# Performance work log

Measured on AMD Instinct MI355X. Metric: run time of the kernel, lower is better.

## Reference

```python
import jax, jax.numpy as jnp
import numpy as np

H = 16          # num_heads
W = 256         # sliding window size
LN_EPS = 1e-6
ROPE_BASE = 10000.0


def layer_norm(x, g, b):
    m = jnp.mean(x, axis=-1, keepdims=True)
    v = jnp.mean((x - m) ** 2, axis=-1, keepdims=True)
    return (x - m) * jax.lax.rsqrt(v + LN_EPS) * g + b


def rope(x):
    # x: [B, S, H, hd]; rotate-half RoPE
    S, hd = x.shape[1], x.shape[-1]
    inv_freq = 1.0 / (ROPE_BASE ** (jnp.arange(0, hd, 2, dtype=jnp.float32) / hd))
    ang = jnp.arange(S, dtype=jnp.float32)[:, None] * inv_freq[None, :]  # [S, hd/2]
    cos = jnp.concatenate([jnp.cos(ang), jnp.cos(ang)], axis=-1)[None, :, None, :]
    sin = jnp.concatenate([jnp.sin(ang), jnp.sin(ang)], axis=-1)[None, :, None, :]
    x1, x2 = jnp.split(x, 2, axis=-1)
    rot = jnp.concatenate([-x2, x1], axis=-1)
    return x * cos + rot * sin


def setup_inputs() -> dict:
    key = jax.random.key(0)
    ks = jax.random.split(key, 12)
    B, S, D, I = 2, 2048, 1024, 4096
    s = 0.02
    return {
        "hidden_states": jax.random.normal(ks[0], (B, S, D), jnp.float32),
        "wq": jax.random.normal(ks[1], (D, D), jnp.float32) * s,
        "wk": jax.random.normal(ks[2], (D, D), jnp.float32) * s,
        "wv": jax.random.normal(ks[3], (D, D), jnp.float32) * s,
        "wo": jax.random.normal(ks[4], (D, D), jnp.float32) * s,
        "w1": jax.random.normal(ks[5], (D, I), jnp.float32) * s,
        "w2": jax.random.normal(ks[6], (I, D), jnp.float32) * s,
        "w3": jax.random.normal(ks[7], (D, I), jnp.float32) * s,
        "ln1_g": jnp.ones((D,), jnp.float32),
        "ln1_b": jnp.zeros((D,), jnp.float32),
        "ln2_g": jnp.ones((D,), jnp.float32),
        "ln2_b": jnp.zeros((D,), jnp.float32),
    }


def reference(hidden_states, wq, wk, wv, wo, w1, w2, w3, ln1_g, ln1_b, ln2_g, ln2_b):
    B, S, D = hidden_states.shape
    hd = D // H

    # --- attention sub-block ---
    residual = hidden_states
    x = layer_norm(hidden_states, ln1_g, ln1_b)
    q = (x @ wq).reshape(B, S, H, hd)
    k = (x @ wk).reshape(B, S, H, hd)
    v = (x @ wv).reshape(B, S, H, hd)
    q, k = rope(q), rope(k)

    scores = jnp.einsum("bqhd,bkhd->bhqk", q, k) / jnp.sqrt(jnp.float32(hd))
    idx = jnp.arange(S)
    rel = idx[:, None] - idx[None, :]          # i - j
    mask = (rel >= 0) & (rel < W)              # causal sliding window
    scores = jnp.where(mask[None, None], scores, jnp.float32(-1e9))
    attn = jax.nn.softmax(scores, axis=-1)
    ctx = jnp.einsum("bhqk,bkhd->bqhd", attn, v).reshape(B, S, D)
    hidden_states = residual + ctx @ wo

    # --- SwiGLU MLP sub-block ---
    residual = hidden_states
    x = layer_norm(hidden_states, ln2_g, ln2_b)
    mlp = (jax.nn.silu(x @ w1) * (x @ w3)) @ w2
    return residual + mlp
```

## Files before the change

### kernel.cpp

```cpp
#include <hip/hip_runtime.h>
#include <hip/hip_bf16.h>

typedef __bf16 bf16_t;
typedef __bf16 bf16x4 __attribute__((ext_vector_type(4)));
typedef __bf16 bf16x8 __attribute__((ext_vector_type(8)));
typedef float f32x4 __attribute__((ext_vector_type(4)));
typedef float f32x16 __attribute__((ext_vector_type(16)));

#define LN_EPS 1e-6f

__device__ __forceinline__ void gl2lds16(const void* g, void* l) {
    __builtin_amdgcn_global_load_lds(
        (const __attribute__((address_space(1))) void*)g,
        (__attribute__((address_space(3))) void*)l, 16, 0, 0);
}

__global__ void transpose_cvt_kernel(const float* __restrict__ in, bf16_t* __restrict__ out,
                                     int R, int C) {
    __shared__ float tile[32][33];
    int tx = threadIdx.x & 31;
    int ty = threadIdx.x >> 5;
    int r0 = blockIdx.y * 32;
    int c0 = blockIdx.x * 32;
#pragma unroll
    for (int i = 0; i < 4; i++) {
        int r = ty + i * 8;
        tile[r][tx] = in[(size_t)(r0 + r) * C + (c0 + tx)];
    }
    __syncthreads();
#pragma unroll
    for (int i = 0; i < 4; i++) {
        int r = ty + i * 8;
        out[(size_t)(c0 + r) * R + (r0 + tx)] = (bf16_t)tile[tx][r];
    }
}

__global__ void ln_kernel(const float* __restrict__ x, const float* __restrict__ g,
                          const float* __restrict__ bb, bf16_t* __restrict__ out, int D) {
    int row = blockIdx.x;
    int t = threadIdx.x;
    const float4* xr = reinterpret_cast<const float4*>(x + (size_t)row * D);
    float4 v = xr[t];
    float s = v.x + v.y + v.z + v.w;
    __shared__ float sbuf[4];
    __shared__ float sbuf2[4];
    int wave = t >> 6, lane = t & 63;
#pragma unroll
    for (int o = 32; o > 0; o >>= 1) s += __shfl_xor(s, o);
    if (lane == 0) sbuf[wave] = s;
    __syncthreads();
    float mean = (sbuf[0] + sbuf[1] + sbuf[2] + sbuf[3]) / (float)D;
    float d0 = v.x - mean, d1 = v.y - mean, d2 = v.z - mean, d3 = v.w - mean;
    float sq = d0 * d0 + d1 * d1 + d2 * d2 + d3 * d3;
#pragma unroll
    for (int o = 32; o > 0; o >>= 1) sq += __shfl_xor(sq, o);
    if (lane == 0) sbuf2[wave] = sq;
    __syncthreads();
    float var = (sbuf2[0] + sbuf2[1] + sbuf2[2] + sbuf2[3]) / (float)D;
    float inv = rsqrtf(var + LN_EPS);
    float4 gv = reinterpret_cast<const float4*>(g)[t];
    float4 bv = reinterpret_cast<const float4*>(bb)[t];
    bf16_t* o0 = out + (size_t)row * D + t * 4;
    o0[0] = (bf16_t)(d0 * inv * gv.x + bv.x);
    o0[1] = (bf16_t)(d1 * inv * gv.y + bv.y);
    o0[2] = (bf16_t)(d2 * inv * gv.z + bv.z);
    o0[3] = (bf16_t)(d3 * inv * gv.w + bv.w);
}

#define BM 128
#define BN 128
#define BKK 32

template <int EPI>
__launch_bounds__(256, 2) __global__
void gemm_kernel(const bf16_t* __restrict__ A, const bf16_t* __restrict__ Bt,
                 float* __restrict__ Cf, const float* __restrict__ aux,
                 const bf16_t* __restrict__ auxb, bf16_t* __restrict__ Cb,
                 int M, int N, int K) {
    __shared__ __align__(16) bf16_t As[BM * BKK];
    __shared__ __align__(16) bf16_t Bs[BN * BKK];
    int t = threadIdx.x;
    int lin = blockIdx.y * gridDim.x + blockIdx.x;
    int gmt = gridDim.y;
    int gw = 8 * gmt;
    int grp = lin / gw;
    int rem = lin - grp * gw;
    int bn = grp * 8 + (rem & 7);
    int bm = rem >> 3;
    int m0 = bm * BM;
    int n0 = bn * BN;
    int wave = t >> 6, lane = t & 63;
    int wm = (wave >> 1) * 64, wn = (wave & 1) * 64;
    int lr = lane & 15;
    int quad = lane >> 4;

    int srow = lane >> 2;
    int scol = (lane & 3) * 8;
    const bf16_t* ag = A + (size_t)(m0 + wave * 16 + srow) * K + scol;
    const bf16_t* bg = Bt + (size_t)(n0 + wave * 16 + srow) * K + scol;
    bf16_t* asl = As + wave * 16 * BKK;
    bf16_t* bsl = Bs + wave * 16 * BKK;
    const size_t rowskip = (size_t)64 * K;

    f32x4 acc[4][4];
#pragma unroll
    for (int mi = 0; mi < 4; mi++)
#pragma unroll
        for (int ni = 0; ni < 4; ni++) acc[mi][ni] = 0.f;

    for (int k0 = 0; k0 < K; k0 += BKK) {
        gl2lds16(ag + k0, asl);
        gl2lds16(ag + k0 + rowskip, asl + 64 * BKK);
        gl2lds16(bg + k0, bsl);
        gl2lds16(bg + k0 + rowskip, bsl + 64 * BKK);
        __syncthreads();
        bf16x8 af[4], bfv[4];
#pragma unroll
        for (int mi = 0; mi < 4; mi++)
            af[mi] = *reinterpret_cast<const bf16x8*>(&As[(wm + mi * 16 + lr) * BKK + quad * 8]);
#pragma unroll
        for (int ni = 0; ni < 4; ni++)
            bfv[ni] = *reinterpret_cast<const bf16x8*>(&Bs[(wn + ni * 16 + lr) * BKK + quad * 8]);
#pragma unroll
        for (int mi = 0; mi < 4; mi++)
#pragma unroll
            for (int ni = 0; ni < 4; ni++)
                acc[mi][ni] = __builtin_amdgcn_mfma_f32_16x16x32_bf16(af[mi], bfv[ni],
                                                                      acc[mi][ni], 0, 0, 0);
        __syncthreads();
    }
#pragma unroll
    for (int mi = 0; mi < 4; mi++) {
#pragma unroll
        for (int ni = 0; ni < 4; ni++) {
#pragma unroll
            for (int j = 0; j < 4; j++) {
                int gm = m0 + wm + mi * 16 + quad * 4 + j;
                int gn = n0 + wn + ni * 16 + lr;
                size_t idx = (size_t)gm * N + gn;
                float val = acc[mi][ni][j];
                if constexpr (EPI == 1) {
                    Cf[idx] = val + aux[idx];
                }
            }
        }
    }
}

#define G2_BM 256
#define G2_BN 128
#define G2_BK 32

template <int EPI>
__launch_bounds__(256, 2) __global__
void gemm2_kernel(const bf16_t* __restrict__ A, const bf16_t* __restrict__ Bt,
                  const bf16_t* __restrict__ auxb, bf16_t* __restrict__ Cb,
                  int M, int N, int K, int lda, int ldb) {
    __shared__ __align__(16) bf16_t As[G2_BM * G2_BK];
    __shared__ __align__(16) bf16_t Bs[G2_BN * G2_BK];
    int t = threadIdx.x;
    int wave = t >> 6, lane = t & 63;
    int m0 = blockIdx.x * G2_BM;
    int n0 = blockIdx.y * G2_BN;
    int koff = blockIdx.z * K;

    int sr = lane >> 2;
    int sq = (lane & 3) ^ (sr & 3);
    const bf16_t* ag = A + (size_t)(m0 + 64 * wave + sr) * lda + koff + sq * 8;
    const bf16_t* bg = Bt + (size_t)(n0 + 32 * wave + sr) * ldb + koff + sq * 8;
    bf16_t* asl = As + (64 * wave) * G2_BK;
    bf16_t* bsl = Bs + (32 * wave) * G2_BK;

    f32x16 acc[2][4];
#pragma unroll
    for (int mi = 0; mi < 2; mi++)
#pragma unroll
        for (int ni = 0; ni < 4; ni++) acc[mi][ni] = 0.f;

    int l31 = lane & 31;
    int lh = lane >> 5;
    int lx = lane & 3;

    for (int k0 = 0; k0 < K; k0 += G2_BK) {
#pragma unroll
        for (int i = 0; i < 4; i++)
            gl2lds16(ag + k0 + (size_t)(16 * i) * lda, asl + (16 * i) * G2_BK);
#pragma unroll
        for (int i = 0; i < 2; i++)
            gl2lds16(bg + k0 + (size_t)(16 * i) * ldb, bsl + (16 * i) * G2_BK);
        __syncthreads();
#pragma unroll
        for (int s = 0; s < 2; s++) {
            int q = 2 * s + lh;
            bf16x8 af[2], bfv[4];
#pragma unroll
            for (int mi = 0; mi < 2; mi++) {
                int row = 64 * wave + mi * 32 + l31;
                af[mi] = *reinterpret_cast<const bf16x8*>(&As[row * G2_BK + (q ^ lx) * 8]);
            }
#pragma unroll
            for (int ni = 0; ni < 4; ni++) {
                int row = ni * 32 + l31;
                bfv[ni] = *reinterpret_cast<const bf16x8*>(&Bs[row * G2_BK + (q ^ lx) * 8]);
            }
#pragma unroll
            for (int mi = 0; mi < 2; mi++)
#pragma unroll
                for (int ni = 0; ni < 4; ni++)
                    acc[mi][ni] = __builtin_amdgcn_mfma_f32_32x32x16_bf16(af[mi], bfv[ni],
                                                                          acc[mi][ni], 0, 0, 0);
        }
        __syncthreads();
    }

    if constexpr (EPI == 3) {
        const float kfreq = -0.41524101186f;
        bool do_rope = (n0 < 2048);
#pragma unroll
        for (int mi = 0; mi < 2; mi++) {
#pragma unroll
            for (int reg = 0; reg < 16; reg++) {
                int rrow = (reg & 3) + 8 * (reg >> 2) + 4 * lh;
                int gm = m0 + 64 * wave + mi * 32 + rrow;
                if (do_rope) {
                    float sf = (float)(gm & 2047);
                    float freq = exp2f((float)l31 * kfreq);
                    float ang = sf * freq;
                    float sn, cs;
                    __sincosf(ang, &sn, &cs);
#pragma unroll
                    for (int p = 0; p < 2; p++) {
                        float x1 = acc[mi][2 * p][reg];
                        float x2 = acc[mi][2 * p + 1][reg];
                        size_t idx = (size_t)gm * N + n0 + p * 64 + l31;
                        Cb[idx] = (bf16_t)(x1 * cs - x2 * sn);
                        Cb[idx + 32] = (bf16_t)(x2 * cs + x1 * sn);
                    }
                } else {
#pragma unroll
                    for (int ni = 0; ni < 4; ni++) {
                        size_t idx = (size_t)gm * N + n0 + ni * 32 + l31;
                        Cb[idx] = (bf16_t)acc[mi][ni][reg];
                    }
                }
            }
        }
    } else {
        size_t outoff = (EPI == 5) ? (size_t)blockIdx.z * M * N : 0;
#pragma unroll
        for (int mi = 0; mi < 2; mi++) {
#pragma unroll
            for (int reg = 0; reg < 16; reg++) {
                int rrow = (reg & 3) + 8 * (reg >> 2) + 4 * lh;
                int gm = m0 + 64 * wave + mi * 32 + rrow;
#pragma unroll
                for (int ni = 0; ni < 4; ni++) {
                    int gn = n0 + ni * 32 + l31;
                    size_t idx = (size_t)gm * N + gn;
                    float val = acc[mi][ni][reg];
                    if constexpr (EPI == 2) {
                        float a = (float)auxb[idx];
                        float sl = a / (1.0f + __expf(-a));
                        Cb[idx] = (bf16_t)(sl * val);
                    } else if constexpr (EPI == 4) {
                        Cb[idx] = (bf16_t)val;
                    } else if constexpr (EPI == 5) {
                        Cb[outoff + idx] = (bf16_t)val;
                    }
                }
            }
        }
    }
}

__global__ void reduce4_kernel(const bf16_t* __restrict__ p, const float* __restrict__ hid,
                               float* __restrict__ out, int n4) {
    int i = blockIdx.x * 256 + threadIdx.x;
    if (i >= n4) return;
    size_t i4 = (size_t)i * 4;
    float4 h = *reinterpret_cast<const float4*>(hid + i4);
    const size_t stride = (size_t)4096 * 1024;
#pragma unroll
    for (int c = 0; c < 4; c++) {
        bf16x4 a = *reinterpret_cast<const bf16x4*>(p + c * stride + i4);
        h.x += (float)a[0];
        h.y += (float)a[1];
        h.z += (float)a[2];
        h.w += (float)a[3];
    }
    *reinterpret_cast<float4*>(out + i4) = h;
}

__global__ void transpose_v_kernel(const bf16_t* __restrict__ v, bf16_t* __restrict__ vt,
                                   int S, int stride) {
    __shared__ bf16_t tile[64][66];
    int t = threadIdx.x;
    int s0 = blockIdx.x * 64;
    int h = blockIdx.y, b = blockIdx.z;
#pragma unroll
    for (int i = 0; i < 2; i++) {
        int c = t + i * 256;
        int ss = c >> 3, d8 = (c & 7) * 8;
        bf16x8 val = *reinterpret_cast<const bf16x8*>(
            &v[(size_t)(b * S + s0 + ss) * stride + h * 64 + d8]);
#pragma unroll
        for (int jj = 0; jj < 8; jj++) tile[ss][d8 + jj] = val[jj];
    }
    __syncthreads();
#pragma unroll
    for (int i = 0; i < 2; i++) {
        int c = t + i * 256;
        int d = c >> 3, s8 = (c & 7) * 8;
        bf16x8 o;
#pragma unroll
        for (int jj = 0; jj < 8; jj++) o[jj] = tile[s8 + jj][d];
        *reinterpret_cast<bf16x8*>(&vt[(((size_t)(b * 16 + h)) * 64 + d) * S + s0 + s8]) = o;
    }
}

#define PSTR 40
#define QKVS 3072
__global__ __launch_bounds__(256, 2) void attn_kernel(const bf16_t* __restrict__ qkv,
                                                      const bf16_t* __restrict__ vt,
                                                      bf16_t* __restrict__ ctx, int S) {
    __shared__ __align__(16) bf16_t Pbuf[4][16 * PSTR];
    int t = threadIdx.x;
    int wave = t >> 6, lane = t & 63;
    int col = lane & 15, quad = lane >> 4;
    int h = blockIdx.y, b = blockIdx.z;
    int q0 = blockIdx.x * 64 + wave * 16;

    const bf16_t* qrow = qkv + (size_t)(b * S + q0 + col) * QKVS + h * 64;
    bf16x8 aq0 = *reinterpret_cast<const bf16x8*>(qrow + quad * 8);
    bf16x8 aq1 = *reinterpret_cast<const bf16x8*>(qrow + 32 + quad * 8);

    int jbase = q0 - 256;
    f32x4 sc[18];
#pragma unroll
    for (int kt = 0; kt < 18; kt++) {
        int j = jbase + kt * 16 + col;
        int jc = j < 0 ? 0 : (j > S - 1 ? S - 1 : j);
        const bf16_t* krow = qkv + (size_t)(b * S + jc) * QKVS + 1024 + h * 64;
        bf16x8 bk0 = *reinterpret_cast<const bf16x8*>(krow + quad * 8);
        bf16x8 bk1 = *reinterpret_cast<const bf16x8*>(krow + 32 + quad * 8);
        f32x4 c0 = {0.f, 0.f, 0.f, 0.f};
        c0 = __builtin_amdgcn_mfma_f32_16x16x32_bf16(aq0, bk0, c0, 0, 0, 0);
        c0 = __builtin_amdgcn_mfma_f32_16x16x32_bf16(aq1, bk1, c0, 0, 0, 0);
        sc[kt] = c0;
    }
#pragma unroll
    for (int kt = 0; kt < 18; kt++) {
#pragma unroll
        for (int jj = 0; jj < 4; jj++) {
            int qq = quad * 4 + jj;
            int j = jbase + kt * 16 + col;
            int rel = (q0 + qq) - j;
            bool ok = (j >= 0) && (rel >= 0) && (rel < 256);
            sc[kt][jj] = ok ? sc[kt][jj] * 0.125f : -1e30f;
        }
    }
    float sminv[4];
#pragma unroll
    for (int jj = 0; jj < 4; jj++) {
        float m = -1e30f;
#pragma unroll
        for (int kt = 0; kt < 18; kt++) m = fmaxf(m, sc[kt][jj]);
#pragma unroll
        for (int o = 1; o < 16; o <<= 1) m = fmaxf(m, __shfl_xor(m, o));
        float s = 0.f;
#pragma unroll
        for (int kt = 0; kt < 18; kt++) {
            float p = __expf(sc[kt][jj] - m);
            sc[kt][jj] = p;
            s += p;
        }
#pragma unroll
        for (int o = 1; o < 16; o <<= 1) s += __shfl_xor(s, o);
        sminv[jj] = 1.0f / s;
    }
    f32x4 o[4];
#pragma unroll
    for (int n = 0; n < 4; n++) o[n] = 0.f;
    bf16_t* myP = Pbuf[wave];
    const bf16_t* vplane = vt + ((size_t)(b * 16 + h)) * 64 * S;
#pragma unroll
    for (int c = 0; c < 9; c++) {
#pragma unroll
        for (int half = 0; half < 2; half++) {
            int kt = 2 * c + half;
#pragma unroll
            for (int jj = 0; jj < 4; jj++) {
                int qq = quad * 4 + jj;
                myP[qq * PSTR + half * 16 + col] = (bf16_t)(sc[kt][jj] * sminv[jj]);
            }
        }
        bf16x8 ap = *reinterpret_cast<const bf16x8*>(myP + col * PSTR + quad * 8);
        int key0 = jbase + c * 32 + quad * 8;
        int kc = key0 < 0 ? 0 : (key0 > S - 8 ? S - 8 : key0);
#pragma unroll
        for (int n = 0; n < 4; n++) {
            bf16x8 bv = *reinterpret_cast<const bf16x8*>(vplane + ((size_t)(n * 16 + col)) * S + kc);
            o[n] = __builtin_amdgcn_mfma_f32_16x16x32_bf16(ap, bv, o[n], 0, 0, 0);
        }
    }
#pragma unroll
    for (int n = 0; n < 4; n++)
#pragma unroll
        for (int jj = 0; jj < 4; jj++) {
            int qq = quad * 4 + jj;
            ctx[((size_t)(b * S + q0 + qq) * 16 + h) * 64 + n * 16 + col] = (bf16_t)o[n][jj];
        }
}

extern "C" void kernel_launch(void* const* d_in, const int* in_sizes, int n_in,
                              void* d_out, int out_size, void* d_ws, size_t ws_size,
                              hipStream_t stream) {
    const float* hs   = (const float*)d_in[0];
    const float* wq   = (const float*)d_in[1];
    const float* wk   = (const float*)d_in[2];
    const float* wv   = (const float*)d_in[3];
    const float* wo   = (const float*)d_in[4];
    const float* w1   = (const float*)d_in[5];
    const float* w2   = (const float*)d_in[6];
    const float* w3   = (const float*)d_in[7];
    const float* ln1g = (const float*)d_in[8];
    const float* ln1b = (const float*)d_in[9];
    const float* ln2g = (const float*)d_in[10];
    const float* ln2b = (const float*)d_in[11];
    float* out = (float*)d_out;

    const int B = 2, S = 2048, D = 1024, I = 4096;
    const int BS = B * S;

    char* ws = (char*)d_ws;
    const size_t MB = 1024 * 1024;
    bf16_t* wq_t = (bf16_t*)(ws + 0 * MB);
    bf16_t* wk_t = (bf16_t*)(ws + 2 * MB);
    bf16_t* wv_t = (bf16_t*)(ws + 4 * MB);
    bf16_t* wo_t = (bf16_t*)(ws + 6 * MB);
    bf16_t* w1_t = (bf16_t*)(ws + 8 * MB);
    bf16_t* w3_t = (bf16_t*)(ws + 16 * MB);
    bf16_t* w2_t = (bf16_t*)(ws + 24 * MB);
    bf16_t* x_b  = (bf16_t*)(ws + 32 * MB);
    float*  hid  = (float*)(ws + 40 * MB);
    bf16_t* x2_b = (bf16_t*)(ws + 56 * MB);
    bf16_t* qkvb = (bf16_t*)(ws + 64 * MB);
    bf16_t* vt   = (bf16_t*)(ws + 88 * MB);
    bf16_t* ctxb = (bf16_t*)(ws + 96 * MB);
    bf16_t* h1b  = (bf16_t*)(ws + 64 * MB);
    bf16_t* hbuf = (bf16_t*)(ws + 96 * MB);
    bf16_t* pker = (bf16_t*)(ws + 64 * MB);

    dim3 tb(256);
    transpose_cvt_kernel<<<dim3(D / 32, D / 32), tb, 0, stream>>>(wq, wq_t, D, D);
    transpose_cvt_kernel<<<dim3(D / 32, D / 32), tb, 0, stream>>>(wk, wk_t, D, D);
    transpose_cvt_kernel<<<dim3(D / 32, D / 32), tb, 0, stream>>>(wv, wv_t, D, D);
    transpose_cvt_kernel<<<dim3(D / 32, D / 32), tb, 0, stream>>>(wo, wo_t, D, D);
    transpose_cvt_kernel<<<dim3(I / 32, D / 32), tb, 0, stream>>>(w1, w1_t, D, I);
    transpose_cvt_kernel<<<dim3(I / 32, D / 32), tb, 0, stream>>>(w3, w3_t, D, I);
    transpose_cvt_kernel<<<dim3(D / 32, I / 32), tb, 0, stream>>>(w2, w2_t, I, D);

    ln_kernel<<<BS, tb, 0, stream>>>(hs, ln1g, ln1b, x_b, D);

    gemm2_kernel<3><<<dim3(BS / G2_BM, 3072 / G2_BN), tb, 0, stream>>>(
        x_b, wq_t, nullptr, qkvb, BS, 3072, D, D, D);

    transpose_v_kernel<<<dim3(S / 64, 16, B), tb, 0, stream>>>(qkvb + 2048, vt, S, QKVS);

    attn_kernel<<<dim3(S / 64, 16, B), tb, 0, stream>>>(qkvb, vt, ctxb, S);

    gemm_kernel<1><<<dim3(D / BN, BS / BM), tb, 0, stream>>>(ctxb, wo_t, hid, hs, nullptr,
                                                             nullptr, BS, D, D);

    ln_kernel<<<BS, tb, 0, stream>>>(hid, ln2g, ln2b, x2_b, D);

    gemm2_kernel<4><<<dim3(BS / G2_BM, I / G2_BN), tb, 0, stream>>>(
        x2_b, w1_t, nullptr, h1b, BS, I, D, D, D);
    gemm2_kernel<2><<<dim3(BS / G2_BM, I / G2_BN), tb, 0, stream>>>(
        x2_b, w3_t, h1b, hbuf, BS, I, D, D, D);

    gemm2_kernel<5><<<dim3(BS / G2_BM, D / G2_BN, 4), tb, 0, stream>>>(
        hbuf, w2_t, nullptr, pker, BS, D, 1024, I, I);
    reduce4_kernel<<<dim3(BS * D / 4 / 256), tb, 0, stream>>>(pker, hid, out, BS * D / 4);
}
```

Before: 421.6 us.

## Replace bf16 GEMM with 256x256 double-buffered 8-wave kernel using 16x16 MFMA

Replaces the 256x128, single-buffered, 4-wave GEMM with a 256x256 tile, BK=64, 8-wave kernel. It double-buffers LDS and prefetches the next K tile in halves, interleaved with four MFMA quadrants separated by barriers, and raises wave priority around the MFMA bursts. The larger tile and the prefetch are meant to raise arithmetic intensity and hide global-load latency. In exchange it uses 128KB of LDS per block, which limits occupancy, adds many barriers per iteration, and produces fewer blocks for the N=1024 GEMMs, which may underfill the CUs.

```diff
diff --git a/kernel.cpp b/kernel.cpp
--- a/kernel.cpp
+++ b/kernel.cpp
@@ -5,7 +5,6 @@
 typedef __bf16 bf16x4 __attribute__((ext_vector_type(4)));
 typedef __bf16 bf16x8 __attribute__((ext_vector_type(8)));
 typedef float f32x4 __attribute__((ext_vector_type(4)));
-typedef float f32x16 __attribute__((ext_vector_type(16)));
 
 #define LN_EPS 1e-6f
 
@@ -13,6 +12,12 @@
     __builtin_amdgcn_global_load_lds(
         (const __attribute__((address_space(1))) void*)g,
         (__attribute__((address_space(3))) void*)l, 16, 0, 0);
+}
+
+__device__ __forceinline__ void block_sync() {
+    __asm__ __volatile__("" ::: "memory");
+    __builtin_amdgcn_s_barrier();
+    __asm__ __volatile__("" ::: "memory");
 }
 
 __global__ void transpose_cvt_kernel(const float* __restrict__ in, bf16_t* __restrict__ out,
@@ -147,100 +152,183 @@
     }
 }
 
-#define G2_BM 256
-#define G2_BN 128
-#define G2_BK 32
+#define G3_BM 256
+#define G3_BN 256
+#define G3_BK 64
+
+__device__ __forceinline__ void stage_half(const bf16_t* g, int ld, bf16_t* l,
+                                           int wave, int lane) {
+#pragma unroll
+    for (int i = 0; i < 2; i++) {
+        int lidx = (wave * 2 + i) * 64 + lane;
+        int row = lidx >> 3;
+        int ss = (lidx & 7) ^ (row & 7);
+        gl2lds16(g + (size_t)row * ld + ss * 8, l + (wave * 2 + i) * 512);
+    }
+}
+
+template <int MH, int NHB>
+__device__ __forceinline__ void mfma_quad(f32x4 (&acc)[8][4], const bf16x8 (&af)[4][2],
+                                          const bf16x8 (&bf)[2][2]) {
+#pragma unroll
+    for (int f = 0; f < 4; f++)
+#pragma unroll
+        for (int n = 0; n < 2; n++)
+#pragma unroll
+            for (int s = 0; s < 2; s++)
+                acc[MH * 4 + f][NHB * 2 + n] = __builtin_amdgcn_mfma_f32_16x16x32_bf16(
+                    af[f][s], bf[n][s], acc[MH * 4 + f][NHB * 2 + n], 0, 0, 0);
+}
 
 template <int EPI>
-__launch_bounds__(256, 2) __global__
-void gemm2_kernel(const bf16_t* __restrict__ A, const bf16_t* __restrict__ Bt,
+__launch_bounds__(512, 2) __global__
+void gemm3_kernel(const bf16_t* __restrict__ A, const bf16_t* __restrict__ Bt,
                   const bf16_t* __restrict__ auxb, bf16_t* __restrict__ Cb,
                   int M, int N, int K, int lda, int ldb) {
-    __shared__ __align__(16) bf16_t As[G2_BM * G2_BK];
-    __shared__ __align__(16) bf16_t Bs[G2_BN * G2_BK];
-    int t = threadIdx.x;
-    int wave = t >> 6, lane = t & 63;
-    int m0 = blockIdx.x * G2_BM;
-    int n0 = blockIdx.y * G2_BN;
-    int koff = blockIdx.z * K;
-
-    int sr = lane >> 2;
-    int sq = (lane & 3) ^ (sr & 3);
-    const bf16_t* ag = A + (size_t)(m0 + 64 * wave + sr) * lda + koff + sq * 8;
-    const bf16_t* bg = Bt + (size_t)(n0 + 32 * wave + sr) * ldb + koff + sq * 8;
-    bf16_t* asl = As + (64 * wave) * G2_BK;
-    bf16_t* bsl = Bs + (32 * wave) * G2_BK;
-
-    f32x16 acc[2][4];
-#pragma unroll
-    for (int mi = 0; mi < 2; mi++)
+    __shared__ __align__(16) bf16_t As[2 * 256 * 64];
+    __shared__ __align__(16) bf16_t Bs[2 * 256 * 64];
+    const int t = threadIdx.x;
+    const int wave = t >> 6, lane = t & 63;
+    const int wm = wave >> 2, wn = wave & 3;
+    const int lr = lane & 15, quad = lane >> 4;
+    const int m0 = blockIdx.x * G3_BM;
+    const int n0 = blockIdx.y * G3_BN;
+    const int koff = blockIdx.z * K;
+
+    const bf16_t* Ag = A + (size_t)m0 * lda + koff;
+    const bf16_t* Bg = Bt + (size_t)n0 * ldb + koff;
+
+    int aoff[4][2], b0off[2][2], b1off[2][2];
+    const int brow = (wn & 1) * 64;
+#pragma unroll
+    for (int f = 0; f < 4; f++)
+#pragma unroll
+        for (int s = 0; s < 2; s++) {
+            int row = f * 16 + lr;
+            aoff[f][s] = row * 64 + (((s * 4 + quad) ^ (row & 7)) << 3);
+        }
+#pragma unroll
+    for (int f = 0; f < 2; f++)
+#pragma unroll
+        for (int s = 0; s < 2; s++) {
+            int r0 = brow + f * 16 + lr;
+            int r1 = brow + 32 + f * 16 + lr;
+            b0off[f][s] = r0 * 64 + (((s * 4 + quad) ^ (r0 & 7)) << 3);
+            b1off[f][s] = r1 * 64 + (((s * 4 + quad) ^ (r1 & 7)) << 3);
+        }
+
+    f32x4 acc[8][4];
+#pragma unroll
+    for (int mi = 0; mi < 8; mi++)
 #pragma unroll
         for (int ni = 0; ni < 4; ni++) acc[mi][ni] = 0.f;
 
-    int l31 = lane & 31;
-    int lh = lane >> 5;
-    int lx = lane & 3;
-
-    for (int k0 = 0; k0 < K; k0 += G2_BK) {
-#pragma unroll
-        for (int i = 0; i < 4; i++)
-            gl2lds16(ag + k0 + (size_t)(16 * i) * lda, asl + (16 * i) * G2_BK);
-#pragma unroll
-        for (int i = 0; i < 2; i++)
-            gl2lds16(bg + k0 + (size_t)(16 * i) * ldb, bsl + (16 * i) * G2_BK);
-        __syncthreads();
-#pragma unroll
-        for (int s = 0; s < 2; s++) {
-            int q = 2 * s + lh;
-            bf16x8 af[2], bfv[4];
-#pragma unroll
-            for (int mi = 0; mi < 2; mi++) {
-                int row = 64 * wave + mi * 32 + l31;
-                af[mi] = *reinterpret_cast<const bf16x8*>(&As[row * G2_BK + (q ^ lx) * 8]);
-            }
-#pragma unroll
-            for (int ni = 0; ni < 4; ni++) {
-                int row = ni * 32 + l31;
-                bfv[ni] = *reinterpret_cast<const bf16x8*>(&Bs[row * G2_BK + (q ^ lx) * 8]);
-            }
-#pragma unroll
-            for (int mi = 0; mi < 2; mi++)
-#pragma unroll
-                for (int ni = 0; ni < 4; ni++)
-                    acc[mi][ni] = __builtin_amdgcn_mfma_f32_32x32x16_bf16(af[mi], bfv[ni],
-                                                                          acc[mi][ni], 0, 0, 0);
-        }
-        __syncthreads();
-    }
-
+    stage_half(Ag, lda, As, wave, lane);
+    stage_half(Ag + (size_t)128 * lda, lda, As + 8192, wave, lane);
+    stage_half(Bg, ldb, Bs, wave, lane);
+    stage_half(Bg + (size_t)128 * ldb, ldb, Bs + 8192, wave, lane);
+    __asm__ __volatile__("s_waitcnt vmcnt(0)" ::: "memory");
+    block_sync();
+
+    const int NT = K >> 6;
+    bf16x8 afr[4][2], bf0[2][2], bf1[2][2];
+
+    for (int tt = 0; tt < NT; ++tt) {
+        const bf16_t* Ab = As + (tt & 1) * 16384 + wm * 8192;
+        const bf16_t* Bb = Bs + (tt & 1) * 16384 + (wn >> 1) * 8192;
+        bf16_t* Asn = As + ((tt + 1) & 1) * 16384;
+        bf16_t* Bsn = Bs + ((tt + 1) & 1) * 16384;
+        const bool pf = (tt + 1 < NT);
+        const int kn = (tt + 1) << 6;
+
+#pragma unroll
+        for (int f = 0; f < 4; f++)
+#pragma unroll
+            for (int s = 0; s < 2; s++)
+                afr[f][s] = *reinterpret_cast<const bf16x8*>(Ab + aoff[f][s]);
+#pragma unroll
+        for (int f = 0; f < 2; f++)
+#pragma unroll
+            for (int s = 0; s < 2; s++)
+                bf0[f][s] = *reinterpret_cast<const bf16x8*>(Bb + b0off[f][s]);
+        if (pf) {
+            stage_half(Ag + kn, lda, Asn, wave, lane);
+            stage_half(Ag + (size_t)128 * lda + kn, lda, Asn + 8192, wave, lane);
+        }
+        block_sync();
+        __asm__ __volatile__("s_waitcnt lgkmcnt(0)" ::: "memory");
+        __builtin_amdgcn_sched_barrier(0);
+        __builtin_amdgcn_s_setprio(1);
+        mfma_quad<0, 0>(acc, afr, bf0);
+        __builtin_amdgcn_s_setprio(0);
+        block_sync();
+
+#pragma unroll
+        for (int f = 0; f < 2; f++)
+#pragma unroll
+            for (int s = 0; s < 2; s++)
+                bf1[f][s] = *reinterpret_cast<const bf16x8*>(Bb + b1off[f][s]);
+        if (pf) {
+            stage_half(Bg + kn, ldb, Bsn, wave, lane);
+            stage_half(Bg + (size_t)128 * ldb + kn, ldb, Bsn + 8192, wave, lane);
+        }
+        block_sync();
+        __asm__ __volatile__("s_waitcnt lgkmcnt(0)" ::: "memory");
+        __builtin_amdgcn_sched_barrier(0);
+        __builtin_amdgcn_s_setprio(1);
+        mfma_quad<0, 1>(acc, afr, bf1);
+        __builtin_amdgcn_s_setprio(0);
+        block_sync();
+
+#pragma unroll
+        for (int f = 0; f < 4; f++)
+#pragma unroll
+            for (int s = 0; s < 2; s++)
+                afr[f][s] = *reinterpret_cast<const bf16x8*>(Ab + 4096 + aoff[f][s]);
+        block_sync();
+        __asm__ __volatile__("s_waitcnt lgkmcnt(0)" ::: "memory");
+        __builtin_amdgcn_sched_barrier(0);
+        __builtin_amdgcn_s_setprio(1);
+        mfma_quad<1, 1>(acc, afr, bf1);
+        __builtin_amdgcn_s_setprio(0);
+        block_sync();
+
+        __builtin_amdgcn_s_setprio(1);
+        mfma_quad<1, 0>(acc, afr, bf0);
+        __builtin_amdgcn_s_setprio(0);
+        __asm__ __volatile__("s_waitcnt vmcnt(0)" ::: "memory");
+        block_sync();
+    }
+
+    const int cw = n0 + wn * 64;
     if constexpr (EPI == 3) {
         const float kfreq = -0.41524101186f;
-        bool do_rope = (n0 < 2048);
-#pragma unroll
-        for (int mi = 0; mi < 2; mi++) {
-#pragma unroll
-            for (int reg = 0; reg < 16; reg++) {
-                int rrow = (reg & 3) + 8 * (reg >> 2) + 4 * lh;
-                int gm = m0 + 64 * wave + mi * 32 + rrow;
+        bool do_rope = (cw < 2048);
+#pragma unroll
+        for (int mi = 0; mi < 8; mi++) {
+#pragma unroll
+            for (int j = 0; j < 4; j++) {
+                int gm = m0 + wm * 128 + mi * 16 + quad * 4 + j;
                 if (do_rope) {
-                    float sf = (float)(gm & 2047);
-                    float freq = exp2f((float)l31 * kfreq);
-                    float ang = sf * freq;
-                    float sn, cs;
-                    __sincosf(ang, &sn, &cs);
+                    float pos = (float)(gm & 2047);
 #pragma unroll
                     for (int p = 0; p < 2; p++) {
-                        float x1 = acc[mi][2 * p][reg];
-                        float x2 = acc[mi][2 * p + 1][reg];
-                        size_t idx = (size_t)gm * N + n0 + p * 64 + l31;
+                        float x1 = acc[mi][p][j];
+                        float x2 = acc[mi][p + 2][j];
+                        int d = p * 16 + lr;
+                        float freq = exp2f((float)d * kfreq);
+                        float ang = pos * freq;
+                        float sn, cs;
+                        __sincosf(ang, &sn, &cs);
+                        size_t idx = (size_t)gm * N + cw + d;
                         Cb[idx] = (bf16_t)(x1 * cs - x2 * sn);
                         Cb[idx + 32] = (bf16_t)(x2 * cs + x1 * sn);
                     }
                 } else {
 #pragma unroll
                     for (int ni = 0; ni < 4; ni++) {
-                        size_t idx = (size_t)gm * N + n0 + ni * 32 + l31;
-                        Cb[idx] = (bf16_t)acc[mi][ni][reg];
+                        size_t idx = (size_t)gm * N + cw + ni * 16 + lr;
+                        Cb[idx] = (bf16_t)acc[mi][ni][j];
                     }
                 }
             }
@@ -248,16 +336,15 @@
     } else {
         size_t outoff = (EPI == 5) ? (size_t)blockIdx.z * M * N : 0;
 #pragma unroll
-        for (int mi = 0; mi < 2; mi++) {
-#pragma unroll
-            for (int reg = 0; reg < 16; reg++) {
-                int rrow = (reg & 3) + 8 * (reg >> 2) + 4 * lh;
-                int gm = m0 + 64 * wave + mi * 32 + rrow;
-#pragma unroll
-                for (int ni = 0; ni < 4; ni++) {
-                    int gn = n0 + ni * 32 + l31;
+        for (int mi = 0; mi < 8; mi++)
+#pragma unroll
+            for (int ni = 0; ni < 4; ni++)
+#pragma unroll
+                for (int j = 0; j < 4; j++) {
+                    int gm = m0 + wm * 128 + mi * 16 + quad * 4 + j;
+                    int gn = cw + ni * 16 + lr;
                     size_t idx = (size_t)gm * N + gn;
-                    float val = acc[mi][ni][reg];
+                    float val = acc[mi][ni][j];
                     if constexpr (EPI == 2) {
                         float a = (float)auxb[idx];
                         float sl = a / (1.0f + __expf(-a));
@@ -268,8 +355,6 @@
                         Cb[outoff + idx] = (bf16_t)val;
                     }
                 }
-            }
-        }
     }
 }
 
@@ -452,6 +537,7 @@
     bf16_t* pker = (bf16_t*)(ws + 64 * MB);
 
     dim3 tb(256);
+    dim3 tb3(512);
     transpose_cvt_kernel<<<dim3(D / 32, D / 32), tb, 0, stream>>>(wq, wq_t, D, D);
     transpose_cvt_kernel<<<dim3(D / 32, D / 32), tb, 0, stream>>>(wk, wk_t, D, D);
     transpose_cvt_kernel<<<dim3(D / 32, D / 32), tb, 0, stream>>>(wv, wv_t, D, D);
@@ -462,7 +548,7 @@
 
     ln_kernel<<<BS, tb, 0, stream>>>(hs, ln1g, ln1b, x_b, D);
 
-    gemm2_kernel<3><<<dim3(BS / G2_BM, 3072 / G2_BN), tb, 0, stream>>>(
+    gemm3_kernel<3><<<dim3(BS / G3_BM, 3072 / G3_BN), tb3, 0, stream>>>(
         x_b, wq_t, nullptr, qkvb, BS, 3072, D, D, D);
 
     transpose_v_kernel<<<dim3(S / 64, 16, B), tb, 0, stream>>>(qkvb + 2048, vt, S, QKVS);
@@ -474,12 +560,12 @@
 
     ln_kernel<<<BS, tb, 0, stream>>>(hid, ln2g, ln2b, x2_b, D);
 
-    gemm2_kernel<4><<<dim3(BS / G2_BM, I / G2_BN), tb, 0, stream>>>(
+    gemm3_kernel<4><<<dim3(BS / G3_BM, I / G3_BN), tb3, 0, stream>>>(
         x2_b, w1_t, nullptr, h1b, BS, I, D, D, D);
-    gemm2_kernel<2><<<dim3(BS / G2_BM, I / G2_BN), tb, 0, stream>>>(
+    gemm3_kernel<2><<<dim3(BS / G3_BM, I / G3_BN), tb3, 0, stream>>>(
         x2_b, w3_t, h1b, hbuf, BS, I, D, D, D);
 
-    gemm2_kernel<5><<<dim3(BS / G2_BM, D / G2_BN, 4), tb, 0, stream>>>(
+    gemm3_kernel<5><<<dim3(BS / G3_BM, D / G3_BN, 4), tb3, 0, stream>>>(
         hbuf, w2_t, nullptr, pker, BS, D, 1024, I, I);
     reduce4_kernel<<<dim3(BS * D / 4 / 256), tb, 0, stream>>>(pker, hid, out, BS * D / 4);
 }
```

Measured after the change: 414.8 us. No clear change (-1.6%).

## Unify GEMMs into 128x128 BK64 swizzled kernel with XCD-aware tile mapping

Applied to the files above, without the earlier changes.

Replaces the two GEMM kernels with a single 128x128 tile kernel using a K-step of 64 and an XOR-swizzled LDS layout to avoid bank conflicts. It also remaps workgroups round-robin across 8 groups, apparently to spread tiles over the chiplets. The split-K for the down projection drops from 4 to 2 partial slices, with a matching 2-way reduce. The RoPE epilogue is rewritten for the 16x16 MFMA fragment layout. This trades the 32x32 MFMA with larger M tiles for more LDS per block and more blocks, which may change occupancy and data reuse.

```diff
diff --git a/kernel.cpp b/kernel.cpp
--- a/kernel.cpp
+++ b/kernel.cpp
@@ -5,7 +5,6 @@
 typedef __bf16 bf16x4 __attribute__((ext_vector_type(4)));
 typedef __bf16 bf16x8 __attribute__((ext_vector_type(8)));
 typedef float f32x4 __attribute__((ext_vector_type(4)));
-typedef float f32x16 __attribute__((ext_vector_type(16)));
 
 #define LN_EPS 1e-6f
 
@@ -67,40 +66,47 @@
     o0[3] = (bf16_t)(d3 * inv * gv.w + bv.w);
 }
 
-#define BM 128
-#define BN 128
-#define BKK 32
+#define G4_BK 64
 
 template <int EPI>
 __launch_bounds__(256, 2) __global__
-void gemm_kernel(const bf16_t* __restrict__ A, const bf16_t* __restrict__ Bt,
-                 float* __restrict__ Cf, const float* __restrict__ aux,
-                 const bf16_t* __restrict__ auxb, bf16_t* __restrict__ Cb,
-                 int M, int N, int K) {
-    __shared__ __align__(16) bf16_t As[BM * BKK];
-    __shared__ __align__(16) bf16_t Bs[BN * BKK];
-    int t = threadIdx.x;
-    int lin = blockIdx.y * gridDim.x + blockIdx.x;
-    int gmt = gridDim.y;
-    int gw = 8 * gmt;
-    int grp = lin / gw;
-    int rem = lin - grp * gw;
-    int bn = grp * 8 + (rem & 7);
-    int bm = rem >> 3;
-    int m0 = bm * BM;
-    int n0 = bn * BN;
-    int wave = t >> 6, lane = t & 63;
-    int wm = (wave >> 1) * 64, wn = (wave & 1) * 64;
-    int lr = lane & 15;
-    int quad = lane >> 4;
-
-    int srow = lane >> 2;
-    int scol = (lane & 3) * 8;
-    const bf16_t* ag = A + (size_t)(m0 + wave * 16 + srow) * K + scol;
-    const bf16_t* bg = Bt + (size_t)(n0 + wave * 16 + srow) * K + scol;
-    bf16_t* asl = As + wave * 16 * BKK;
-    bf16_t* bsl = Bs + wave * 16 * BKK;
-    const size_t rowskip = (size_t)64 * K;
+void gemm4_kernel(const bf16_t* __restrict__ A, const bf16_t* __restrict__ Bt,
+                  float* __restrict__ Cf, const float* __restrict__ aux,
+                  const bf16_t* __restrict__ auxb, bf16_t* __restrict__ Cb,
+                  int M, int N, int K, int lda, int ldb) {
+    __shared__ __align__(16) bf16_t As[128 * G4_BK];
+    __shared__ __align__(16) bf16_t Bs[128 * G4_BK];
+    const int t = threadIdx.x;
+    const int wave = t >> 6, lane = t & 63;
+    const int lr = lane & 15, quad = lane >> 4;
+    const int wm = (wave >> 1) * 64, wn = (wave & 1) * 64;
+
+    const int gx = gridDim.x, gy = gridDim.y;
+    const int nwg = gx * gy;
+    const int lin = blockIdx.y * gx + blockIdx.x;
+    const int qch = nwg >> 3;
+    const int sw = (lin & 7) * qch + (lin >> 3);
+    const int m0 = (sw / gy) * 128;
+    const int n0 = (sw % gy) * 128;
+    const int koff = blockIdx.z * K;
+
+    const int srow = t >> 3;
+    const int sslot = (t & 7) ^ (srow & 7);
+    const bf16_t* agp = A + (size_t)(m0 + srow) * lda + koff + sslot * 8;
+    const bf16_t* bgp = Bt + (size_t)(n0 + srow) * ldb + koff + sslot * 8;
+    bf16_t* asl = As + t * 8;
+    bf16_t* bsl = Bs + t * 8;
+
+    int aoff[4][2], boff[4][2];
+#pragma unroll
+    for (int f = 0; f < 4; f++)
+#pragma unroll
+        for (int s = 0; s < 2; s++) {
+            int ra = wm + f * 16 + lr;
+            int rb = wn + f * 16 + lr;
+            aoff[f][s] = ra * G4_BK + (((s * 4 + quad) ^ (ra & 7)) << 3);
+            boff[f][s] = rb * G4_BK + (((s * 4 + quad) ^ (rb & 7)) << 3);
+        }
 
     f32x4 acc[4][4];
 #pragma unroll
@@ -108,139 +114,62 @@
 #pragma unroll
         for (int ni = 0; ni < 4; ni++) acc[mi][ni] = 0.f;
 
-    for (int k0 = 0; k0 < K; k0 += BKK) {
-        gl2lds16(ag + k0, asl);
-        gl2lds16(ag + k0 + rowskip, asl + 64 * BKK);
-        gl2lds16(bg + k0, bsl);
-        gl2lds16(bg + k0 + rowskip, bsl + 64 * BKK);
+    for (int k0 = 0; k0 < K; k0 += G4_BK) {
+#pragma unroll
+        for (int i = 0; i < 4; i++)
+            gl2lds16(agp + k0 + (size_t)(32 * i) * lda, asl + i * 2048);
+#pragma unroll
+        for (int i = 0; i < 4; i++)
+            gl2lds16(bgp + k0 + (size_t)(32 * i) * ldb, bsl + i * 2048);
         __syncthreads();
-        bf16x8 af[4], bfv[4];
-#pragma unroll
-        for (int mi = 0; mi < 4; mi++)
-            af[mi] = *reinterpret_cast<const bf16x8*>(&As[(wm + mi * 16 + lr) * BKK + quad * 8]);
-#pragma unroll
-        for (int ni = 0; ni < 4; ni++)
-            bfv[ni] = *reinterpret_cast<const bf16x8*>(&Bs[(wn + ni * 16 + lr) * BKK + quad * 8]);
-#pragma unroll
-        for (int mi = 0; mi < 4; mi++)
+#pragma unroll
+        for (int s = 0; s < 2; s++) {
+            bf16x8 af[4], bfv[4];
+#pragma unroll
+            for (int mi = 0; mi < 4; mi++)
+                af[mi] = *reinterpret_cast<const bf16x8*>(&As[aoff[mi][s]]);
 #pragma unroll
             for (int ni = 0; ni < 4; ni++)
-                acc[mi][ni] = __builtin_amdgcn_mfma_f32_16x16x32_bf16(af[mi], bfv[ni],
-                                                                      acc[mi][ni], 0, 0, 0);
+                bfv[ni] = *reinterpret_cast<const bf16x8*>(&Bs[boff[ni][s]]);
+#pragma unroll
+            for (int mi = 0; mi < 4; mi++)
+#pragma unroll
+                for (int ni = 0; ni < 4; ni++)
+                    acc[mi][ni] = __builtin_amdgcn_mfma_f32_16x16x32_bf16(af[mi], bfv[ni],
+                                                                          acc[mi][ni], 0, 0, 0);
+        }
         __syncthreads();
     }
-#pragma unroll
-    for (int mi = 0; mi < 4; mi++) {
-#pragma unroll
-        for (int ni = 0; ni < 4; ni++) {
+
+    if constexpr (EPI == 3) {
+        const float kfreq = -0.41524101186f;
+        const int cw = n0 + wn;
+        bool do_rope = (cw < 2048);
+#pragma unroll
+        for (int mi = 0; mi < 4; mi++) {
 #pragma unroll
             for (int j = 0; j < 4; j++) {
                 int gm = m0 + wm + mi * 16 + quad * 4 + j;
-                int gn = n0 + wn + ni * 16 + lr;
-                size_t idx = (size_t)gm * N + gn;
-                float val = acc[mi][ni][j];
-                if constexpr (EPI == 1) {
-                    Cf[idx] = val + aux[idx];
-                }
-            }
-        }
-    }
-}
-
-#define G2_BM 256
-#define G2_BN 128
-#define G2_BK 32
-
-template <int EPI>
-__launch_bounds__(256, 2) __global__
-void gemm2_kernel(const bf16_t* __restrict__ A, const bf16_t* __restrict__ Bt,
-                  const bf16_t* __restrict__ auxb, bf16_t* __restrict__ Cb,
-                  int M, int N, int K, int lda, int ldb) {
-    __shared__ __align__(16) bf16_t As[G2_BM * G2_BK];
-    __shared__ __align__(16) bf16_t Bs[G2_BN * G2_BK];
-    int t = threadIdx.x;
-    int wave = t >> 6, lane = t & 63;
-    int m0 = blockIdx.x * G2_BM;
-    int n0 = blockIdx.y * G2_BN;
-    int koff = blockIdx.z * K;
-
-    int sr = lane >> 2;
-    int sq = (lane & 3) ^ (sr & 3);
-    const bf16_t* ag = A + (size_t)(m0 + 64 * wave + sr) * lda + koff + sq * 8;
-    const bf16_t* bg = Bt + (size_t)(n0 + 32 * wave + sr) * ldb + koff + sq * 8;
-    bf16_t* asl = As + (64 * wave) * G2_BK;
-    bf16_t* bsl = Bs + (32 * wave) * G2_BK;
-
-    f32x16 acc[2][4];
-#pragma unroll
-    for (int mi = 0; mi < 2; mi++)
-#pragma unroll
-        for (int ni = 0; ni < 4; ni++) acc[mi][ni] = 0.f;
-
-    int l31 = lane & 31;
-    int lh = lane >> 5;
-    int lx = lane & 3;
-
-    for (int k0 = 0; k0 < K; k0 += G2_BK) {
-#pragma unroll
-        for (int i = 0; i < 4; i++)
-            gl2lds16(ag + k0 + (size_t)(16 * i) * lda, asl + (16 * i) * G2_BK);
-#pragma unroll
-        for (int i = 0; i < 2; i++)
-            gl2lds16(bg + k0 + (size_t)(16 * i) * ldb, bsl + (16 * i) * G2_BK);
-        __syncthreads();
-#pragma unroll
-        for (int s = 0; s < 2; s++) {
-            int q = 2 * s + lh;
-            bf16x8 af[2], bfv[4];
-#pragma unroll
-            for (int mi = 0; mi < 2; mi++) {
-                int row = 64 * wave + mi * 32 + l31;
-                af[mi] = *reinterpret_cast<const bf16x8*>(&As[row * G2_BK + (q ^ lx) * 8]);
-            }
-#pragma unroll
-            for (int ni = 0; ni < 4; ni++) {
-                int row = ni * 32 + l31;
-                bfv[ni] = *reinterpret_cast<const bf16x8*>(&Bs[row * G2_BK + (q ^ lx) * 8]);
-            }
-#pragma unroll
-            for (int mi = 0; mi < 2; mi++)
-#pragma unroll
-                for (int ni = 0; ni < 4; ni++)
-                    acc[mi][ni] = __builtin_amdgcn_mfma_f32_32x32x16_bf16(af[mi], bfv[ni],
-                                                                          acc[mi][ni], 0, 0, 0);
-        }
-        __syncthreads();
-    }
-
-    if constexpr (EPI == 3) {
-        const float kfreq = -0.41524101186f;
-        bool do_rope = (n0 < 2048);
-#pragma unroll
-        for (int mi = 0; mi < 2; mi++) {
-#pragma unroll
-            for (int reg = 0; reg < 16; reg++) {
-                int rrow = (reg & 3) + 8 * (reg >> 2) + 4 * lh;
-                int gm = m0 + 64 * wave + mi * 32 + rrow;
                 if (do_rope) {
-                    float sf = (float)(gm & 2047);
-                    float freq = exp2f((float)l31 * kfreq);
-                    float ang = sf * freq;
-                    float sn, cs;
-                    __sincosf(ang, &sn, &cs);
+                    float pos = (float)(gm & 2047);
 #pragma unroll
                     for (int p = 0; p < 2; p++) {
-                        float x1 = acc[mi][2 * p][reg];
-                        float x2 = acc[mi][2 * p + 1][reg];
-                        size_t idx = (size_t)gm * N + n0 + p * 64 + l31;
+                        float x1 = acc[mi][p][j];
+                        float x2 = acc[mi][p + 2][j];
+                        int d = p * 16 + lr;
+                        float freq = exp2f((float)d * kfreq);
+                        float ang = pos * freq;
+                        float sn, cs;
+                        __sincosf(ang, &sn, &cs);
+                        size_t idx = (size_t)gm * N + cw + d;
                         Cb[idx] = (bf16_t)(x1 * cs - x2 * sn);
                         Cb[idx + 32] = (bf16_t)(x2 * cs + x1 * sn);
                     }
                 } else {
 #pragma unroll
                     for (int ni = 0; ni < 4; ni++) {
-                        size_t idx = (size_t)gm * N + n0 + ni * 32 + l31;
-                        Cb[idx] = (bf16_t)acc[mi][ni][reg];
+                        size_t idx = (size_t)gm * N + cw + ni * 16 + lr;
+                        Cb[idx] = (bf16_t)acc[mi][ni][j];
                     }
                 }
             }
@@ -248,17 +177,18 @@
     } else {
         size_t outoff = (EPI == 5) ? (size_t)blockIdx.z * M * N : 0;
 #pragma unroll
-        for (int mi = 0; mi < 2; mi++) {
-#pragma unroll
-            for (int reg = 0; reg < 16; reg++) {
-                int rrow = (reg & 3) + 8 * (reg >> 2) + 4 * lh;
-                int gm = m0 + 64 * wave + mi * 32 + rrow;
-#pragma unroll
-                for (int ni = 0; ni < 4; ni++) {
-                    int gn = n0 + ni * 32 + l31;
+        for (int mi = 0; mi < 4; mi++)
+#pragma unroll
+            for (int ni = 0; ni < 4; ni++)
+#pragma unroll
+                for (int j = 0; j < 4; j++) {
+                    int gm = m0 + wm + mi * 16 + quad * 4 + j;
+                    int gn = n0 + wn + ni * 16 + lr;
                     size_t idx = (size_t)gm * N + gn;
-                    float val = acc[mi][ni][reg];
-                    if constexpr (EPI == 2) {
+                    float val = acc[mi][ni][j];
+                    if constexpr (EPI == 1) {
+                        Cf[idx] = val + aux[idx];
+                    } else if constexpr (EPI == 2) {
                         float a = (float)auxb[idx];
                         float sl = a / (1.0f + __expf(-a));
                         Cb[idx] = (bf16_t)(sl * val);
@@ -268,12 +198,10 @@
                         Cb[outoff + idx] = (bf16_t)val;
                     }
                 }
-            }
-        }
-    }
-}
-
-__global__ void reduce4_kernel(const bf16_t* __restrict__ p, const float* __restrict__ hid,
+    }
+}
+
+__global__ void reduce2_kernel(const bf16_t* __restrict__ p, const float* __restrict__ hid,
                                float* __restrict__ out, int n4) {
     int i = blockIdx.x * 256 + threadIdx.x;
     if (i >= n4) return;
@@ -281,7 +209,7 @@
     float4 h = *reinterpret_cast<const float4*>(hid + i4);
     const size_t stride = (size_t)4096 * 1024;
 #pragma unroll
-    for (int c = 0; c < 4; c++) {
+    for (int c = 0; c < 2; c++) {
         bf16x4 a = *reinterpret_cast<const bf16x4*>(p + c * stride + i4);
         h.x += (float)a[0];
         h.y += (float)a[1];
@@ -462,24 +390,24 @@
 
     ln_kernel<<<BS, tb, 0, stream>>>(hs, ln1g, ln1b, x_b, D);
 
-    gemm2_kernel<3><<<dim3(BS / G2_BM, 3072 / G2_BN), tb, 0, stream>>>(
-        x_b, wq_t, nullptr, qkvb, BS, 3072, D, D, D);
+    gemm4_kernel<3><<<dim3(BS / 128, 3072 / 128), tb, 0, stream>>>(
+        x_b, wq_t, nullptr, nullptr, nullptr, qkvb, BS, 3072, D, D, D);
 
     transpose_v_kernel<<<dim3(S / 64, 16, B), tb, 0, stream>>>(qkvb + 2048, vt, S, QKVS);
 
     attn_kernel<<<dim3(S / 64, 16, B), tb, 0, stream>>>(qkvb, vt, ctxb, S);
 
-    gemm_kernel<1><<<dim3(D / BN, BS / BM), tb, 0, stream>>>(ctxb, wo_t, hid, hs, nullptr,
-                                                             nullptr, BS, D, D);
+    gemm4_kernel<1><<<dim3(BS / 128, D / 128), tb, 0, stream>>>(
+        ctxb, wo_t, hid, hs, nullptr, nullptr, BS, D, D, D, D);
 
     ln_kernel<<<BS, tb, 0, stream>>>(hid, ln2g, ln2b, x2_b, D);
 
-    gemm2_kernel<4><<<dim3(BS / G2_BM, I / G2_BN), tb, 0, stream>>>(
-        x2_b, w1_t, nullptr, h1b, BS, I, D, D, D);
-    gemm2_kernel<2><<<dim3(BS / G2_BM, I / G2_BN), tb, 0, stream>>>(
-        x2_b, w3_t, h1b, hbuf, BS, I, D, D, D);
-
-    gemm2_kernel<5><<<dim3(BS / G2_BM, D / G2_BN, 4), tb, 0, stream>>>(
-        hbuf, w2_t, nullptr, pker, BS, D, 1024, I, I);
-    reduce4_kernel<<<dim3(BS * D / 4 / 256), tb, 0, stream>>>(pker, hid, out, BS * D / 4);
-}
+    gemm4_kernel<4><<<dim3(BS / 128, I / 128), tb, 0, stream>>>(
+        x2_b, w1_t, nullptr, nullptr, nullptr, h1b, BS, I, D, D, D);
+    gemm4_kernel<2><<<dim3(BS / 128, I / 128), tb, 0, stream>>>(
+        x2_b, w3_t, nullptr, nullptr, h1b, hbuf, BS, I, D, D, D);
+
+    gemm4_kernel<5><<<dim3(BS / 128, D / 128, 2), tb, 0, stream>>>(
+        hbuf, w2_t, nullptr, nullptr, nullptr, pker, BS, D, 2048, I, I);
+    reduce2_kernel<<<dim3(BS * D / 4 / 256), tb, 0, stream>>>(pker, hid, out, BS * D / 4);
+}
```

New measurement: 388.8 us. -7.8%, faster.
